# Kernel optimization log

Measured on AMD Instinct MI355X. Metric: run time of the kernel, lower is better.

The kernel has to match this reference:

```python
import jax, jax.numpy as jnp
import numpy as np

N_QUBITS = 6      # 4 data + 2 ancilla
N_DATA = 4
N_LAYERS = 4
N_GROUPS = 8
DIM = 2 ** N_QUBITS  # 64 statevector amplitudes (real: RY + CNOT keep state real)
GN_GROUPS = 32
EPS = 1e-5


def _cnot_ring_perm():
    # CNOT(q, q+1 mod n) ring applied sequentially; compose into one basis permutation.
    n = N_QUBITS
    f = np.arange(DIM)
    for c in range(n):
        t = (c + 1) % n
        cbit = (f >> (n - 1 - c)) & 1
        f = np.where(cbit == 1, f ^ (1 << (n - 1 - t)), f)
    # new_state[f[i]] = old_state[i]  =>  new = old[finv]
    finv = np.empty(DIM, dtype=np.int64)
    finv[f] = np.arange(DIM)
    return jnp.asarray(finv)


def _zsign():
    i = np.arange(DIM)[:, None]
    q = np.arange(N_DATA)[None, :]
    return jnp.asarray(1.0 - 2.0 * ((i >> (N_QUBITS - 1 - q)) & 1), dtype=jnp.float32)


PERM = _cnot_ring_perm()
ZSIGN = _zsign()


def _group_norm(x, gamma, beta):
    B, C, H, W = x.shape
    xg = x.reshape(B, GN_GROUPS, C // GN_GROUPS, H, W)
    mu = xg.mean(axis=(2, 3, 4), keepdims=True)
    var = xg.var(axis=(2, 3, 4), keepdims=True)
    xn = ((xg - mu) * jax.lax.rsqrt(var + EPS)).reshape(B, C, H, W)
    return xn * gamma[None, :, None, None] + beta[None, :, None, None]


def _apply_ry(state, half_angle, q):
    # state: [B,H,W,G,64]; half_angle: [B,H,W,G]; RY = [[c,-s],[s,c]] on qubit q
    pre, post = 2 ** q, 2 ** (N_QUBITS - 1 - q)
    s = state.reshape(state.shape[:-1] + (pre, 2, post))
    c = jnp.cos(half_angle)[..., None, None]
    sn = jnp.sin(half_angle)[..., None, None]
    a0, a1 = s[..., 0, :], s[..., 1, :]
    new = jnp.stack([c * a0 - sn * a1, sn * a0 + c * a1], axis=-2)
    return new.reshape(state.shape)


def _forward(x, emb, gamma, beta, w_in, b_in, theta, w_style, b_style, w_out, b_out):
    B, C, H, W = x.shape
    h = _group_norm(x, gamma, beta)                       # norm0
    emb_a = emb * jax.nn.sigmoid(emb)                     # SiLU(emb)
    # 1x1 projection to per-group data-qubit rotation angles: [B,H,W,G,4]
    ang = jnp.einsum('oc,bchw->bohw', w_in, h) + b_in[None, :, None, None]
    ang = ang.reshape(B, N_GROUPS, N_DATA, H, W).transpose(0, 3, 4, 1, 2)
    # style modulation of circuit parameters: [B,G,L,Q]
    style = (emb_a @ w_style.T + b_style).reshape(B, N_GROUPS, N_LAYERS, N_QUBITS)
    # init |0...0> per pixel per group
    state = jnp.zeros((B, H, W, N_GROUPS, DIM), x.dtype).at[..., 0].set(1.0)
    for l in range(N_LAYERS):
        for q in range(N_QUBITS):
            a = theta[:, l, q][None, None, None, :] + style[:, :, l, q][:, None, None, :]
            if q < N_DATA:                                # data reuploading each layer
                a = a + ang[..., q]
            state = _apply_ry(state, 0.5 * a, q)
        state = state[..., PERM]                          # CNOT ring entangler
    probs = state * state
    meas = probs @ ZSIGN                                  # [B,H,W,G,4] <Z> on data qubits
    meas = meas.transpose(0, 3, 4, 1, 2).reshape(B, N_GROUPS * N_DATA, H, W)
    out = jnp.einsum('oc,bchw->bohw', w_out, meas) + b_out[None, :, None, None]
    return out + x                                        # residual


def setup_inputs() -> dict:
    key = jax.random.key(0)
    ks = jax.random.split(key, 6)
    B, C, H, W, E = 16, 256, 32, 32, 512
    return {
        'x': jax.random.normal(ks[0], (B, C, H, W), jnp.float32),
        'emb': jax.random.normal(ks[1], (B, E), jnp.float32),
        'gamma': jnp.ones((C,), jnp.float32),
        'beta': jnp.zeros((C,), jnp.float32),
        'w_in': jax.random.normal(ks[2], (32, C), jnp.float32) * 0.1,
        'b_in': jnp.zeros((32,), jnp.float32),
        'theta': jax.random.normal(ks[3], (N_GROUPS, N_LAYERS, N_QUBITS), jnp.float32) * 0.5,
        'w_style': jax.random.normal(ks[4], (N_GROUPS * N_LAYERS * N_QUBITS, E), jnp.float32) * 0.02,
        'b_style': jnp.zeros((N_GROUPS * N_LAYERS * N_QUBITS,), jnp.float32),
        'w_out': jax.random.normal(ks[5], (C, 32), jnp.float32) * 0.05,
        'b_out': jnp.zeros((C,), jnp.float32),
    }


def reference(x, emb, gamma, beta, w_in, b_in, theta, w_style, b_style, w_out, b_out):
    return _forward(x, emb, gamma, beta, w_in, b_in, theta, w_style, b_style, w_out, b_out)
```

## Files before the change

### kernel.cpp

```cpp
#include <hip/hip_runtime.h>
#include <math.h>

#define NB 16
#define NC 256
#define NHW 1024
#define NE 512
#define NDQ 4
#define NLQ 4
#define NQB 6
#define QDIM 64
#define PIX 32
#define HSS 264

typedef float v2f __attribute__((ext_vector_type(2)));
typedef float f32x4 __attribute__((ext_vector_type(4)));
typedef short bf16x8 __attribute__((ext_vector_type(8)));

__device__ __forceinline__ short f2bf(float v) {
    unsigned u = __builtin_bit_cast(unsigned, v);
    u += 0x7FFFu + ((u >> 16) & 1u);
    return (short)(u >> 16);
}

constexpr int fwd1(int i) {
    int r = i;
    for (int c = 0; c < NQB; ++c) {
        int t = (c + 1) % NQB;
        if ((r >> (NQB - 1 - c)) & 1) r ^= 1 << (NQB - 1 - t);
    }
    return r;
}
constexpr int fwdl(int s, int l) { for (int i = 0; i < l; ++i) s = fwd1(s); return s; }
constexpr int parity6(int x) { x ^= x >> 4; x ^= x >> 2; x ^= x >> 1; return x & 1; }

struct GateTab { int M[NLQ][NQB]; int V[NLQ][NQB]; int W[NDQ]; };
constexpr GateTab make_tab() {
    GateTab g{};
    for (int l = 0; l < NLQ; ++l)
        for (int q = 0; q < NQB; ++q) {
            int m = 1 << (NQB - 1 - q);
            for (int x = 0; x < QDIM; ++x) if (fwdl(x, l) == m) { g.M[l][q] = x; break; }
            int V = 0;
            for (int t = 0; t < NQB; ++t) V |= ((fwdl(1 << t, l) >> (NQB - 1 - q)) & 1) << t;
            g.V[l][q] = V;
        }
    for (int d = 0; d < NDQ; ++d) {
        int W = 0;
        for (int t = 0; t < NQB; ++t) W |= ((fwdl(1 << t, NLQ) >> (NQB - 1 - d)) & 1) << t;
        g.W[d] = W;
    }
    return g;
}
constexpr GateTab GT = make_tab();

__global__ __launch_bounds__(256) void k_pre(const float* __restrict__ x,
                                             const float* __restrict__ emb,
                                             const float* __restrict__ w_style,
                                             const float* __restrict__ b_style,
                                             const float* __restrict__ theta,
                                             const float* __restrict__ w_in,
                                             const float* __restrict__ w_out,
                                             const float* __restrict__ gamma,
                                             const float* __restrict__ beta,
                                             float* __restrict__ scs,
                                             float* __restrict__ shs,
                                             float* __restrict__ A,
                                             short* __restrict__ wbf) {
    if (blockIdx.x < 512) {
        int bg = blockIdx.x;
        const float4* xp = (const float4*)(x + (size_t)bg * 8 * NHW);
        float s = 0.f, ss = 0.f;
        for (int i = threadIdx.x; i < 8 * NHW / 4; i += 256) {
            float4 v = xp[i];
            s  += v.x + v.y + v.z + v.w;
            ss += v.x*v.x + v.y*v.y + v.z*v.z + v.w*v.w;
        }
        __shared__ float red0[4], red1[4];
        #pragma unroll
        for (int o = 32; o; o >>= 1) { s += __shfl_down(s, o); ss += __shfl_down(ss, o); }
        int lane = threadIdx.x & 63, w = threadIdx.x >> 6;
        if (lane == 0) { red0[w] = s; red1[w] = ss; }
        __syncthreads();
        if (threadIdx.x == 0) {
            s  = red0[0] + red0[1] + red0[2] + red0[3];
            ss = red1[0] + red1[1] + red1[2] + red1[3];
            float m = s * (1.f / 8192.f);
            float rsv = rsqrtf(ss * (1.f / 8192.f) - m * m + 1e-5f);
            int cbase = (bg & 31) * 8;
            int b = bg >> 5;
            #pragma unroll
            for (int j = 0; j < 8; ++j) {
                int c = cbase + j;
                float sc = rsv * gamma[c];
                scs[b * NC + c] = sc;
                shs[b * NC + c] = fmaf(-m, sc, beta[c]);
            }
        }
    } else if (blockIdx.x < 512 + NB) {
        int b = blockIdx.x - 512;
        __shared__ float es[NE];
        int t = threadIdx.x;
        for (int i = t; i < NE; i += 256) {
            float v = emb[b * NE + i];
            es[i] = v / (1.f + __expf(-v));
        }
        __syncthreads();
        int j0 = t >> 3, sub = t & 7;
        for (int pass = 0; pass < 6; ++pass) {
            int j = pass * 32 + j0;
            const float* wr = w_style + (size_t)j * NE + sub * 64;
            const float* er = es + sub * 64;
            float acc = 0.f;
            #pragma unroll
            for (int i = 0; i < 64; i += 4) {
                float4 w4 = *(const float4*)(wr + i);
                acc = fmaf(w4.x, er[i],   acc);
                acc = fmaf(w4.y, er[i+1], acc);
                acc = fmaf(w4.z, er[i+2], acc);
                acc = fmaf(w4.w, er[i+3], acc);
            }
            acc += __shfl_xor(acc, 1);
            acc += __shfl_xor(acc, 2);
            acc += __shfl_xor(acc, 4);
            if (sub == 0) A[b * 192 + j] = theta[j] + b_style[j] + acc;
        }
    } else {
        for (int i = threadIdx.x; i < 8192; i += 256) wbf[i] = f2bf(w_in[i]);
        for (int i = threadIdx.x; i < 8192; i += 256) wbf[8192 + i] = f2bf(w_out[i]);
    }
}

__global__ __launch_bounds__(256, 2) void k_main(
    const float* __restrict__ x,
    const float* __restrict__ scs,
    const float* __restrict__ shs,
    const float* __restrict__ b_in,
    const float* __restrict__ A,
    const short* __restrict__ w_in_bf,
    const short* __restrict__ w_out_bf,
    const float* __restrict__ b_out,
    float* __restrict__ out) {

    __shared__ short hs[PIX * HSS];
    __shared__ float xs2[NC * PIX];
    __shared__ float as_[PIX * 36];

    int blk = blockIdx.x;
    int b = blk >> 5;
    int pbase = (blk & 31) * PIX;
    int t = threadIdx.x;
    int lane = t & 63, wv = t >> 6;
    int c0 = t >> 3, p4 = (t & 7) * 4;
    int nn = lane & 15, quad = lane >> 4;
    int mt = wv >> 1, nt = wv & 1;

    float4 xr[8];
    #pragma unroll
    for (int k = 0; k < 8; ++k) {
        int c = c0 + 32 * k;
        xr[k] = *(const float4*)(x + (size_t)(b * NC + c) * NHW + pbase + p4);
        *(float4*)(xs2 + c * PIX + p4) = xr[k];
    }

    bf16x8 bfrag[8];
    {
        int o = nt * 16 + nn;
        #pragma unroll
        for (int s = 0; s < 8; ++s)
            bfrag[s] = *(const bf16x8*)(w_in_bf + o * NC + s * 32 + quad * 8);
    }

    float Ar[24];
    {
        int g = t >> 5;
        const float4* Ab4 = (const float4*)(A + b * 192 + g * 24);
        #pragma unroll
        for (int j = 0; j < 6; ++j) {
            float4 a4 = Ab4[j];
            Ar[4*j] = a4.x; Ar[4*j+1] = a4.y; Ar[4*j+2] = a4.z; Ar[4*j+3] = a4.w;
        }
    }

    #pragma unroll
    for (int k = 0; k < 8; ++k) {
        int c = c0 + 32 * k;
        float sc = scs[b * NC + c];
        float sh = shs[b * NC + c];
        float4 v = xr[k];
        hs[(p4 + 0) * HSS + c] = f2bf(fmaf(v.x, sc, sh));
        hs[(p4 + 1) * HSS + c] = f2bf(fmaf(v.y, sc, sh));
        hs[(p4 + 2) * HSS + c] = f2bf(fmaf(v.z, sc, sh));
        hs[(p4 + 3) * HSS + c] = f2bf(fmaf(v.w, sc, sh));
    }
    __syncthreads();

    {
        f32x4 acc = {0.f, 0.f, 0.f, 0.f};
        #pragma unroll
        for (int s = 0; s < 8; ++s) {
            bf16x8 afr = *(const bf16x8*)(hs + (mt * 16 + nn) * HSS + s * 32 + quad * 8);
            acc = __builtin_amdgcn_mfma_f32_16x16x32_bf16(afr, bfrag[s], acc, 0, 0, 0);
        }
        int o = nt * 16 + nn;
        float bi = b_in[o];
        #pragma unroll
        for (int r = 0; r < 4; ++r)
            as_[(mt * 16 + quad * 4 + r) * 36 + o] = acc[r] + bi;
    }

    bf16x8 bfr4[4];
    float  bo4[4];
    #pragma unroll
    for (int ti = 0; ti < 4; ++ti) {
        int c = (wv * 4 + ti) * 16 + nn;
        bfr4[ti] = *(const bf16x8*)(w_out_bf + c * 32 + quad * 8);
        bo4[ti]  = b_out[c];
    }
    __syncthreads();

    {
        int g = t >> 5, p = t & 31;
        float4 angv = *(const float4*)(as_ + p * 36 + g * 4);
        float angp[NDQ] = {angv.x, angv.y, angv.z, angv.w};

        v2f st2[32];
        #pragma unroll
        for (int k = 0; k < 32; ++k) st2[k] = (v2f){0.f, 0.f};
        st2[0].x = 1.f;

        #pragma unroll
        for (int l = 0; l < NLQ; ++l) {
            #pragma unroll
            for (int q = 0; q < NQB; ++q) {
                const int M = GT.M[l][q], V = GT.V[l][q];
                const int KD = M >> 1, SW = M & 1;
                int hh = KD; hh |= hh >> 1; hh |= hh >> 2; hh |= hh >> 4;
                const int HB = hh - (hh >> 1);
                float a = Ar[l * NQB + q] + (q < NDQ ? angp[q] : 0.f);
                float sn, cs;
                __sincosf(0.5f * a, &sn, &cs);
                v2f cs2 = {cs, cs};
                v2f sPP = {sn, sn}, sPM = {sn, -sn}, sMP = {-sn, sn}, sMM = {-sn, -sn};
                auto COV = [&](int i0) -> v2f {
                    bool p0 = parity6(i0 & V), p1 = parity6((i0 + 1) & V);
                    return p0 ? (p1 ? sPP : sPM) : (p1 ? sMP : sMM);
                };
                if (KD == 0) {
                    #pragma unroll
                    for (int k = 0; k < 32; ++k) {
                        v2f ov = __builtin_shufflevector(st2[k], st2[k], 1, 0);
                        st2[k] = __builtin_elementwise_fma(COV(2*k), ov, cs2 * st2[k]);
                    }
                } else {
                    #pragma unroll
                    for (int k = 0; k < 32; ++k) {
                        if (k & HB) continue;
                        int kp = k ^ KD;
                        v2f av = st2[k], bv = st2[kp];
                        v2f am = SW ? __builtin_shufflevector(av, av, 1, 0) : av;
                        v2f bm = SW ? __builtin_shufflevector(bv, bv, 1, 0) : bv;
                        st2[k]  = __builtin_elementwise_fma(COV(2*k),  bm, cs2 * av);
                        st2[kp] = __builtin_elementwise_fma(COV(2*kp), am, cs2 * bv);
                    }
                }
            }
        }

        #pragma unroll
        for (int k = 0; k < 32; ++k) st2[k] = st2[k] * st2[k];
        float md[NDQ];
        #pragma unroll
        for (int d = 0; d < NDQ; ++d) {
            const int W = GT.W[d];
            v2f acc = {0.f, 0.f};
            #pragma unroll
            for (int k = 0; k < 32; ++k) {
                v2f sg = { parity6((2*k)     & W) ? -1.f : 1.f,
                           parity6((2*k + 1) & W) ? -1.f : 1.f };
                acc = __builtin_elementwise_fma(sg, st2[k], acc);
            }
            md[d] = acc.x + acc.y;
        }
        float4 mv = {md[0], md[1], md[2], md[3]};
        *(float4*)(as_ + p * 36 + g * 4) = mv;
    }
    __syncthreads();

    #pragma unroll
    for (int pt = 0; pt < 2; ++pt) {
        float4 m0 = *(const float4*)(as_ + (pt * 16 + nn) * 36 + quad * 8);
        float4 m1 = *(const float4*)(as_ + (pt * 16 + nn) * 36 + quad * 8 + 4);
        bf16x8 afr = { f2bf(m0.x), f2bf(m0.y), f2bf(m0.z), f2bf(m0.w),
                       f2bf(m1.x), f2bf(m1.y), f2bf(m1.z), f2bf(m1.w) };
        #pragma unroll
        for (int ti = 0; ti < 4; ++ti) {
            int c = (wv * 4 + ti) * 16 + nn;
            f32x4 acc = {0.f, 0.f, 0.f, 0.f};
            acc = __builtin_amdgcn_mfma_f32_16x16x32_bf16(afr, bfr4[ti], acc, 0, 0, 0);
            float4 x4 = *(const float4*)(xs2 + c * PIX + pt * 16 + quad * 4);
            float4 r;
            r.x = acc[0] + bo4[ti] + x4.x;
            r.y = acc[1] + bo4[ti] + x4.y;
            r.z = acc[2] + bo4[ti] + x4.z;
            r.w = acc[3] + bo4[ti] + x4.w;
            *(float4*)(out + (size_t)(b * NC + c) * NHW + pbase + pt * 16 + quad * 4) = r;
        }
    }
}

extern "C" void kernel_launch(void* const* d_in, const int* in_sizes, int n_in,
                              void* d_out, int out_size, void* d_ws, size_t ws_size,
                              hipStream_t stream) {
    const float* x       = (const float*)d_in[0];
    const float* emb     = (const float*)d_in[1];
    const float* gamma   = (const float*)d_in[2];
    const float* beta    = (const float*)d_in[3];
    const float* w_in    = (const float*)d_in[4];
    const float* b_in    = (const float*)d_in[5];
    const float* theta   = (const float*)d_in[6];
    const float* w_style = (const float*)d_in[7];
    const float* b_style = (const float*)d_in[8];
    const float* w_out   = (const float*)d_in[9];
    const float* b_out   = (const float*)d_in[10];
    float* out = (float*)d_out;

    float* ws  = (float*)d_ws;
    float* scs = ws;
    float* shs = ws + 4096;
    float* A   = ws + 8192;
    short* wbf = (short*)(ws + 12288);

    k_pre<<<512 + NB + 1, 256, 0, stream>>>(x, emb, w_style, b_style, theta,
                                            w_in, w_out, gamma, beta,
                                            scs, shs, A, wbf);
    k_main<<<NB * 32, 256, 0, stream>>>(x, scs, shs, b_in, A,
                                        wbf, wbf + 8192, b_out, out);
}
```

Measured before the change: 119.0 us.

## Fuse prepass and main kernel into one cooperative launch with grid sync

Merges the GroupNorm-statistics, style-projection and weight-conversion prepass into the main kernel. A cooperative grid-wide barrier separates the two phases, and the x tile is loaded into shared memory before the barrier. This removes one kernel launch and the launch gap between them. It also lets each block's statistics read overlap with its tile load. The shared x buffer gains padding (stride 36) to reduce bank conflicts. If the cooperative launch fails, the code falls back to the two-kernel path. Grid sync adds barrier cost and requires all 512 blocks to be co-resident.

After: 191.3 us. +60.7%, slower.

```diff
diff --git a/kernel.cpp b/kernel.cpp
--- a/kernel.cpp
+++ b/kernel.cpp
@@ -1,4 +1,5 @@
 #include <hip/hip_runtime.h>
+#include <hip/hip_cooperative_groups.h>
 #include <math.h>
 
 #define NB 16
@@ -11,6 +12,7 @@
 #define QDIM 64
 #define PIX 32
 #define HSS 264
+#define XSS 36
 
 typedef float v2f __attribute__((ext_vector_type(2)));
 typedef float f32x4 __attribute__((ext_vector_type(4)));
@@ -53,114 +55,29 @@
 }
 constexpr GateTab GT = make_tab();
 
-__global__ __launch_bounds__(256) void k_pre(const float* __restrict__ x,
-                                             const float* __restrict__ emb,
-                                             const float* __restrict__ w_style,
-                                             const float* __restrict__ b_style,
-                                             const float* __restrict__ theta,
-                                             const float* __restrict__ w_in,
-                                             const float* __restrict__ w_out,
-                                             const float* __restrict__ gamma,
-                                             const float* __restrict__ beta,
-                                             float* __restrict__ scs,
-                                             float* __restrict__ shs,
-                                             float* __restrict__ A,
-                                             short* __restrict__ wbf) {
-    if (blockIdx.x < 512) {
-        int bg = blockIdx.x;
-        const float4* xp = (const float4*)(x + (size_t)bg * 8 * NHW);
-        float s = 0.f, ss = 0.f;
-        for (int i = threadIdx.x; i < 8 * NHW / 4; i += 256) {
-            float4 v = xp[i];
-            s  += v.x + v.y + v.z + v.w;
-            ss += v.x*v.x + v.y*v.y + v.z*v.z + v.w*v.w;
-        }
-        __shared__ float red0[4], red1[4];
-        #pragma unroll
-        for (int o = 32; o; o >>= 1) { s += __shfl_down(s, o); ss += __shfl_down(ss, o); }
-        int lane = threadIdx.x & 63, w = threadIdx.x >> 6;
-        if (lane == 0) { red0[w] = s; red1[w] = ss; }
-        __syncthreads();
-        if (threadIdx.x == 0) {
-            s  = red0[0] + red0[1] + red0[2] + red0[3];
-            ss = red1[0] + red1[1] + red1[2] + red1[3];
-            float m = s * (1.f / 8192.f);
-            float rsv = rsqrtf(ss * (1.f / 8192.f) - m * m + 1e-5f);
-            int cbase = (bg & 31) * 8;
-            int b = bg >> 5;
-            #pragma unroll
-            for (int j = 0; j < 8; ++j) {
-                int c = cbase + j;
-                float sc = rsv * gamma[c];
-                scs[b * NC + c] = sc;
-                shs[b * NC + c] = fmaf(-m, sc, beta[c]);
-            }
-        }
-    } else if (blockIdx.x < 512 + NB) {
-        int b = blockIdx.x - 512;
-        __shared__ float es[NE];
-        int t = threadIdx.x;
-        for (int i = t; i < NE; i += 256) {
-            float v = emb[b * NE + i];
-            es[i] = v / (1.f + __expf(-v));
-        }
-        __syncthreads();
-        int j0 = t >> 3, sub = t & 7;
-        for (int pass = 0; pass < 6; ++pass) {
-            int j = pass * 32 + j0;
-            const float* wr = w_style + (size_t)j * NE + sub * 64;
-            const float* er = es + sub * 64;
-            float acc = 0.f;
-            #pragma unroll
-            for (int i = 0; i < 64; i += 4) {
-                float4 w4 = *(const float4*)(wr + i);
-                acc = fmaf(w4.x, er[i],   acc);
-                acc = fmaf(w4.y, er[i+1], acc);
-                acc = fmaf(w4.z, er[i+2], acc);
-                acc = fmaf(w4.w, er[i+3], acc);
-            }
-            acc += __shfl_xor(acc, 1);
-            acc += __shfl_xor(acc, 2);
-            acc += __shfl_xor(acc, 4);
-            if (sub == 0) A[b * 192 + j] = theta[j] + b_style[j] + acc;
-        }
-    } else {
-        for (int i = threadIdx.x; i < 8192; i += 256) wbf[i] = f2bf(w_in[i]);
-        for (int i = threadIdx.x; i < 8192; i += 256) wbf[8192 + i] = f2bf(w_out[i]);
-    }
-}
-
-__global__ __launch_bounds__(256, 2) void k_main(
-    const float* __restrict__ x,
-    const float* __restrict__ scs,
-    const float* __restrict__ shs,
-    const float* __restrict__ b_in,
-    const float* __restrict__ A,
-    const short* __restrict__ w_in_bf,
-    const short* __restrict__ w_out_bf,
-    const float* __restrict__ b_out,
-    float* __restrict__ out) {
-
-    __shared__ short hs[PIX * HSS];
-    __shared__ float xs2[NC * PIX];
-    __shared__ float as_[PIX * 36];
-
-    int blk = blockIdx.x;
-    int b = blk >> 5;
-    int pbase = (blk & 31) * PIX;
-    int t = threadIdx.x;
+struct Smem {
+    short hs[PIX * HSS];
+    float xs2[NC * XSS];
+    float as_[PIX * 36];
+};
+
+__device__ __forceinline__ void phaseB(Smem& sm, const float4* xr, int b, int pbase, int t,
+                                       const float* __restrict__ scs,
+                                       const float* __restrict__ shs,
+                                       const float* __restrict__ b_in,
+                                       const float* __restrict__ A,
+                                       const short* __restrict__ w_in_bf,
+                                       const short* __restrict__ w_out_bf,
+                                       const float* __restrict__ b_out,
+                                       float* __restrict__ out) {
+    short* hs  = sm.hs;
+    float* xs2 = sm.xs2;
+    float* as_ = sm.as_;
+
     int lane = t & 63, wv = t >> 6;
     int c0 = t >> 3, p4 = (t & 7) * 4;
     int nn = lane & 15, quad = lane >> 4;
     int mt = wv >> 1, nt = wv & 1;
-
-    float4 xr[8];
-    #pragma unroll
-    for (int k = 0; k < 8; ++k) {
-        int c = c0 + 32 * k;
-        xr[k] = *(const float4*)(x + (size_t)(b * NC + c) * NHW + pbase + p4);
-        *(float4*)(xs2 + c * PIX + p4) = xr[k];
-    }
 
     bf16x8 bfrag[8];
     {
@@ -297,7 +214,7 @@
             int c = (wv * 4 + ti) * 16 + nn;
             f32x4 acc = {0.f, 0.f, 0.f, 0.f};
             acc = __builtin_amdgcn_mfma_f32_16x16x32_bf16(afr, bfr4[ti], acc, 0, 0, 0);
-            float4 x4 = *(const float4*)(xs2 + c * PIX + pt * 16 + quad * 4);
+            float4 x4 = *(const float4*)(xs2 + c * XSS + pt * 16 + quad * 4);
             float4 r;
             r.x = acc[0] + bo4[ti] + x4.x;
             r.y = acc[1] + bo4[ti] + x4.y;
@@ -306,6 +223,219 @@
             *(float4*)(out + (size_t)(b * NC + c) * NHW + pbase + pt * 16 + quad * 4) = r;
         }
     }
+}
+
+__global__ __launch_bounds__(256, 2) void k_fused(
+    const float* __restrict__ x,
+    const float* __restrict__ emb,
+    const float* __restrict__ w_style,
+    const float* __restrict__ b_style,
+    const float* __restrict__ theta,
+    const float* __restrict__ w_in,
+    const float* __restrict__ w_out,
+    const float* __restrict__ gamma,
+    const float* __restrict__ beta,
+    const float* __restrict__ b_in,
+    const float* __restrict__ b_out,
+    float* __restrict__ ws,
+    float* __restrict__ out) {
+
+    __shared__ Smem sm;
+    float* scs = ws;
+    float* shs = ws + 4096;
+    float* A   = ws + 8192;
+    short* wbf = (short*)(ws + 12288);
+
+    int blk = blockIdx.x;
+    int t = threadIdx.x;
+    int b = blk >> 5;
+    int pbase = (blk & 31) * PIX;
+
+    float4 xr[8];
+    {
+        int c0 = t >> 3, p4 = (t & 7) * 4;
+        #pragma unroll
+        for (int k = 0; k < 8; ++k) {
+            int c = c0 + 32 * k;
+            xr[k] = *(const float4*)(x + (size_t)(b * NC + c) * NHW + pbase + p4);
+            *(float4*)(sm.xs2 + c * XSS + p4) = xr[k];
+        }
+    }
+
+    {
+        const float4* xp = (const float4*)(x + (size_t)blk * 8 * NHW);
+        float s = 0.f, ss = 0.f;
+        for (int i = t; i < 8 * NHW / 4; i += 256) {
+            float4 v = xp[i];
+            s  += v.x + v.y + v.z + v.w;
+            ss += v.x*v.x + v.y*v.y + v.z*v.z + v.w*v.w;
+        }
+        __shared__ float red0[4], red1[4];
+        #pragma unroll
+        for (int o = 32; o; o >>= 1) { s += __shfl_down(s, o); ss += __shfl_down(ss, o); }
+        int lane = t & 63, w = t >> 6;
+        if (lane == 0) { red0[w] = s; red1[w] = ss; }
+        __syncthreads();
+        if (t == 0) {
+            s  = red0[0] + red0[1] + red0[2] + red0[3];
+            ss = red1[0] + red1[1] + red1[2] + red1[3];
+            float m = s * (1.f / 8192.f);
+            float rsv = rsqrtf(ss * (1.f / 8192.f) - m * m + 1e-5f);
+            int cbase = (blk & 31) * 8;
+            #pragma unroll
+            for (int j = 0; j < 8; ++j) {
+                int c = cbase + j;
+                float sc = rsv * gamma[c];
+                scs[b * NC + c] = sc;
+                shs[b * NC + c] = fmaf(-m, sc, beta[c]);
+            }
+        }
+
+        if (blk < 128) {
+            int sb = blk >> 3, part = blk & 7;
+            float* es = sm.as_;
+            for (int i = t; i < NE; i += 256) {
+                float v = emb[sb * NE + i];
+                es[i] = v / (1.f + __expf(-v));
+            }
+            __syncthreads();
+            int j0 = t >> 3, sub = t & 7;
+            if (j0 < 24) {
+                int j = part * 24 + j0;
+                const float* wr = w_style + (size_t)j * NE + sub * 64;
+                const float* er = es + sub * 64;
+                float acc = 0.f;
+                #pragma unroll
+                for (int i = 0; i < 64; i += 4) {
+                    float4 w4 = *(const float4*)(wr + i);
+                    acc = fmaf(w4.x, er[i],   acc);
+                    acc = fmaf(w4.y, er[i+1], acc);
+                    acc = fmaf(w4.z, er[i+2], acc);
+                    acc = fmaf(w4.w, er[i+3], acc);
+                }
+                acc += __shfl_xor(acc, 1);
+                acc += __shfl_xor(acc, 2);
+                acc += __shfl_xor(acc, 4);
+                if (sub == 0) A[sb * 192 + j] = theta[j] + b_style[j] + acc;
+            }
+        } else if (blk < 144) {
+            int kk = blk - 128;
+            for (int i = t; i < 512; i += 256) {
+                wbf[kk * 512 + i]        = f2bf(w_in[kk * 512 + i]);
+                wbf[8192 + kk * 512 + i] = f2bf(w_out[kk * 512 + i]);
+            }
+        }
+    }
+
+    cooperative_groups::this_grid().sync();
+
+    phaseB(sm, xr, b, pbase, t, scs, shs, b_in, A, wbf, wbf + 8192, b_out, out);
+}
+
+__global__ __launch_bounds__(256) void k_pre(const float* __restrict__ x,
+                                             const float* __restrict__ emb,
+                                             const float* __restrict__ w_style,
+                                             const float* __restrict__ b_style,
+                                             const float* __restrict__ theta,
+                                             const float* __restrict__ w_in,
+                                             const float* __restrict__ w_out,
+                                             const float* __restrict__ gamma,
+                                             const float* __restrict__ beta,
+                                             float* __restrict__ scs,
+                                             float* __restrict__ shs,
+                                             float* __restrict__ A,
+                                             short* __restrict__ wbf) {
+    if (blockIdx.x < 512) {
+        int bg = blockIdx.x;
+        const float4* xp = (const float4*)(x + (size_t)bg * 8 * NHW);
+        float s = 0.f, ss = 0.f;
+        for (int i = threadIdx.x; i < 8 * NHW / 4; i += 256) {
+            float4 v = xp[i];
+            s  += v.x + v.y + v.z + v.w;
+            ss += v.x*v.x + v.y*v.y + v.z*v.z + v.w*v.w;
+        }
+        __shared__ float red0[4], red1[4];
+        #pragma unroll
+        for (int o = 32; o; o >>= 1) { s += __shfl_down(s, o); ss += __shfl_down(ss, o); }
+        int lane = threadIdx.x & 63, w = threadIdx.x >> 6;
+        if (lane == 0) { red0[w] = s; red1[w] = ss; }
+        __syncthreads();
+        if (threadIdx.x == 0) {
+            s  = red0[0] + red0[1] + red0[2] + red0[3];
+            ss = red1[0] + red1[1] + red1[2] + red1[3];
+            float m = s * (1.f / 8192.f);
+            float rsv = rsqrtf(ss * (1.f / 8192.f) - m * m + 1e-5f);
+            int cbase = (bg & 31) * 8;
+            int b = bg >> 5;
+            #pragma unroll
+            for (int j = 0; j < 8; ++j) {
+                int c = cbase + j;
+                float sc = rsv * gamma[c];
+                scs[b * NC + c] = sc;
+                shs[b * NC + c] = fmaf(-m, sc, beta[c]);
+            }
+        }
+    } else if (blockIdx.x < 512 + NB) {
+        int b = blockIdx.x - 512;
+        __shared__ float es[NE];
+        int t = threadIdx.x;
+        for (int i = t; i < NE; i += 256) {
+            float v = emb[b * NE + i];
+            es[i] = v / (1.f + __expf(-v));
+        }
+        __syncthreads();
+        int j0 = t >> 3, sub = t & 7;
+        for (int pass = 0; pass < 6; ++pass) {
+            int j = pass * 32 + j0;
+            const float* wr = w_style + (size_t)j * NE + sub * 64;
+            const float* er = es + sub * 64;
+            float acc = 0.f;
+            #pragma unroll
+            for (int i = 0; i < 64; i += 4) {
+                float4 w4 = *(const float4*)(wr + i);
+                acc = fmaf(w4.x, er[i],   acc);
+                acc = fmaf(w4.y, er[i+1], acc);
+                acc = fmaf(w4.z, er[i+2], acc);
+                acc = fmaf(w4.w, er[i+3], acc);
+            }
+            acc += __shfl_xor(acc, 1);
+            acc += __shfl_xor(acc, 2);
+            acc += __shfl_xor(acc, 4);
+            if (sub == 0) A[b * 192 + j] = theta[j] + b_style[j] + acc;
+        }
+    } else {
+        for (int i = threadIdx.x; i < 8192; i += 256) wbf[i] = f2bf(w_in[i]);
+        for (int i = threadIdx.x; i < 8192; i += 256) wbf[8192 + i] = f2bf(w_out[i]);
+    }
+}
+
+__global__ __launch_bounds__(256, 2) void k_main_fb(
+    const float* __restrict__ x,
+    const float* __restrict__ scs,
+    const float* __restrict__ shs,
+    const float* __restrict__ b_in,
+    const float* __restrict__ A,
+    const short* __restrict__ w_in_bf,
+    const short* __restrict__ w_out_bf,
+    const float* __restrict__ b_out,
+    float* __restrict__ out) {
+
+    __shared__ Smem sm;
+    int blk = blockIdx.x, t = threadIdx.x;
+    int b = blk >> 5;
+    int pbase = (blk & 31) * PIX;
+
+    float4 xr[8];
+    {
+        int c0 = t >> 3, p4 = (t & 7) * 4;
+        #pragma unroll
+        for (int k = 0; k < 8; ++k) {
+            int c = c0 + 32 * k;
+            xr[k] = *(const float4*)(x + (size_t)(b * NC + c) * NHW + pbase + p4);
+            *(float4*)(sm.xs2 + c * XSS + p4) = xr[k];
+        }
+    }
+    phaseB(sm, xr, b, pbase, t, scs, shs, b_in, A, w_in_bf, w_out_bf, b_out, out);
 }
 
 extern "C" void kernel_launch(void* const* d_in, const int* in_sizes, int n_in,
@@ -330,9 +460,21 @@
     float* A   = ws + 8192;
     short* wbf = (short*)(ws + 12288);
 
-    k_pre<<<512 + NB + 1, 256, 0, stream>>>(x, emb, w_style, b_style, theta,
-                                            w_in, w_out, gamma, beta,
-                                            scs, shs, A, wbf);
-    k_main<<<NB * 32, 256, 0, stream>>>(x, scs, shs, b_in, A,
-                                        wbf, wbf + 8192, b_out, out);
-}
+    const float* x_ = x;  const float* emb_ = emb;  const float* wst_ = w_style;
+    const float* bst_ = b_style;  const float* th_ = theta;  const float* wi_ = w_in;
+    const float* wo_ = w_out;  const float* ga_ = gamma;  const float* be_ = beta;
+    const float* bi_ = b_in;  const float* bo_ = b_out;
+    float* ws_ = ws;  float* out_ = out;
+    void* args[] = { &x_, &emb_, &wst_, &bst_, &th_, &wi_, &wo_, &ga_, &be_,
+                     &bi_, &bo_, &ws_, &out_ };
+    hipError_t e = hipLaunchCooperativeKernel((void*)k_fused, dim3(512), dim3(256),
+                                              args, 0, stream);
+    if (e != hipSuccess) {
+        (void)hipGetLastError();
+        k_pre<<<512 + NB + 1, 256, 0, stream>>>(x, emb, w_style, b_style, theta,
+                                                w_in, w_out, gamma, beta,
+                                                scs, shs, A, wbf);
+        k_main_fb<<<NB * 32, 256, 0, stream>>>(x, scs, shs, b_in, A,
+                                               wbf, wbf + 8192, b_out, out);
+    }
+}
```
